# Kernel optimization log

Measured on AMD Instinct MI355X. Metric: run time of the kernel, lower is better.

The kernel has to match this reference:

```python
import jax, jax.numpy as jnp
import numpy as np

SAMPLE_RATE = 44100
NUM_FILTERS = 3
FREQ_LO, FREQ_HI = 100.0, 3000.0
Q_LO, Q_HI = 1.0, 5.0
GAIN_LO, GAIN_HI = -24.0, 24.0


def _center_freqs():
    # power_ratio(i/N, f_lo, f_hi) = f_lo * (f_hi/f_lo)**(i/N)
    return [FREQ_LO * (FREQ_HI / FREQ_LO) ** (i / NUM_FILTERS) for i in range(NUM_FILTERS)]


def setup_inputs() -> dict:
    key = jax.random.key(0)
    k1, k2, k3 = jax.random.split(key, 3)
    audio = jax.random.normal(k1, (32, 441000), dtype=jnp.float32)  # [B, T]
    # Q sampled like power_ratio(u, q_lo, q_hi) = q_lo*(q_hi/q_lo)**u
    u = jax.random.uniform(k2, (NUM_FILTERS,), dtype=jnp.float32)
    qs = Q_LO * (Q_HI / Q_LO) ** u
    gains = jax.random.uniform(k3, (NUM_FILTERS,), dtype=jnp.float32,
                               minval=GAIN_LO, maxval=GAIN_HI)
    return {"audio": audio, "qs": qs, "gains": gains}


def _biquad(x, b0, b1, b2, a1, a2):
    """Direct-form-I biquad over time axis. x: [B, T]; coeffs normalized by a0."""
    B = x.shape[0]
    z = jnp.zeros((B,), x.dtype)

    def step(carry, xn):
        x1, x2, y1, y2 = carry
        yn = b0 * xn + b1 * x1 + b2 * x2 - a1 * y1 - a2 * y2
        return (xn, x1, yn, y1), yn

    _, y = jax.lax.scan(step, (z, z, z, z), x.T)  # scan over T
    return y.T


def _peaking_eq(audio, center_freq, gain, Q):
    # torchaudio.functional.equalizer_biquad coefficients
    w0 = 2.0 * jnp.pi * center_freq / SAMPLE_RATE
    alpha = jnp.sin(w0) / (2.0 * Q)
    A = jnp.exp(gain / 40.0 * jnp.log(10.0))  # 10**(gain/40)
    b0 = 1.0 + alpha * A
    b1 = -2.0 * jnp.cos(w0)
    b2 = 1.0 - alpha * A
    a0 = 1.0 + alpha / A
    a1 = -2.0 * jnp.cos(w0)
    a2 = 1.0 - alpha / A
    return _biquad(audio, b0 / a0, b1 / a0, b2 / a0, a1 / a0, a2 / a0)


def reference(audio, qs, gains):
    cfs = _center_freqs()
    for i in range(NUM_FILTERS):
        audio = _peaking_eq(audio, cfs[i], gains[i], qs[i])
    return audio
```

## Files before the change

### kernel.cpp

```cpp
#include <hip/hip_runtime.h>
#include <math.h>

#define SR      44100.0
#define T_LEN   441000
#define B_ROWS  32
#define NCH     13782
#define GCH     (B_ROWS * NCH)
#define BPR     54
#define NBLK    (B_ROWS * BPR)
#define NMAT    14

#define WS_MAT  0
#define WS_AG   512
#define WS_F    21248

typedef __attribute__((address_space(1))) const void gconst_t;
typedef __attribute__((address_space(3))) void lds_t;
#define GL2LDS(gp, lp) __builtin_amdgcn_global_load_lds((gconst_t*)(gp), (lds_t*)(lp), 16, 0, 0)


#define COMPUTE_COEFS(scoef, dco, qs, gains) do { \
    if (threadIdx.x < 3) { \
      int f = threadIdx.x; \
      double cfq = 100.0 * exp(log(30.0) * (double)f / 3.0); \
      double w0 = 2.0 * M_PI * cfq / SR; \
      double alpha = sin(w0) / (2.0 * (double)qs[f]); \
      double Ag = exp((double)gains[f] * (2.302585092994045684 / 40.0)); \
      double a0 = 1.0 + alpha / Ag; \
      double c0 = (1.0 + alpha * Ag) / a0; \
      double c1 = (-2.0 * cos(w0)) / a0; \
      double c2 = (1.0 - alpha * Ag) / a0; \
      double c3 = c1; \
      double c4 = (1.0 - alpha / Ag) / a0; \
      dco[f*5+0]=c0; dco[f*5+1]=c1; dco[f*5+2]=c2; dco[f*5+3]=c3; dco[f*5+4]=c4; \
      scoef[f*5+0]=(float)c0; scoef[f*5+1]=(float)c1; scoef[f*5+2]=(float)c2; \
      scoef[f*5+3]=(float)c3; scoef[f*5+4]=(float)c4; \
    } \
  } while (0)

#define LOAD_COEFS(cf) \
  const float b00=cf[0],b10=cf[1],b20=cf[2],a10=cf[3],a20=cf[4]; \
  const float b01=cf[5],b11=cf[6],b21=cf[7],a11=cf[8],a21=cf[9]; \
  const float b02=cf[10],b12=cf[11],b22=cf[12],a12=cf[13],a22=cf[14];

#define CASCADE_STEP(xx) do { \
    float y1 = fmaf(b00, (xx), s11); \
    s11 = fmaf(-a10, y1, fmaf(b10, (xx), s21)); \
    s21 = fmaf(-a20, y1, b20 * (xx)); \
    float y2 = fmaf(b01, y1, s12); \
    s12 = fmaf(-a11, y2, fmaf(b11, y1, s22)); \
    s22 = fmaf(-a21, y2, b21 * y1); \
    y3 = fmaf(b02, y2, s13); \
    s13 = fmaf(-a12, y3, fmaf(b12, y2, s23)); \
    s23 = fmaf(-a22, y3, b22 * y2); \
  } while (0)

#define MV6(dst, M, v, add) do { \
    _Pragma("unroll") \
    for (int _i = 0; _i < 6; _i++) { \
      float _s = (add)[_i]; \
      _Pragma("unroll") \
      for (int _k = 0; _k < 6; _k++) _s = fmaf((M)[_i*6+_k], (v)[_k], _s); \
      (dst)[_i] = _s; \
    } \
  } while (0)

__device__ __forceinline__ void mm6d(const double* X, const double* Y, double* Z, int t) {
  if (t < 36) {
    int i = t / 6, j = t % 6;
    double s = 0.0;
    #pragma unroll
    for (int k = 0; k < 6; k++) s += X[i*6+k] * Y[k*6+j];
    Z[t] = s;
  }
}


#define STAGE_AUDIO() do { \
    if (span4 == 512) { \
      _Pragma("unroll") \
      for (int i = 0; i < 8; i++) { \
        int s = (i << 6) + lane; \
        int g = (s & ~7) | ((s & 7) ^ ((s >> 3) & 7)); \
        GL2LDS(xp + g, slab + (i << 8)); \
      } \
    } else { \
      _Pragma("unroll") \
      for (int i = 0; i < 8; i++) { \
        int s = (i << 6) + lane; \
        int g = (s & ~7) | ((s & 7) ^ ((s >> 3) & 7)); \
        if (g < span4) GL2LDS(xp + g, slab + (i << 8)); \
      } \
    } \
  } while (0)


__global__ __launch_bounds__(256) void kA_scan(const float* __restrict__ x,
                                               const float* __restrict__ qs,
                                               const float* __restrict__ gains,
                                               float* __restrict__ ws) {
  __shared__ __align__(16) float lds[4 * 2048];
  __shared__ double Da[36], Db[36];
  __shared__ double dco[15];
  __shared__ float sVm[NMAT][36];
  __shared__ float scoef[16];
  const int tid = threadIdx.x;
  const int wib = tid >> 6, lane = tid & 63;
  const int b = blockIdx.x;
  const int row = b / BPR, jb = b - row * BPR;
  const int wci = (jb << 2) + wib;
  long rowbase = (long)row * T_LEN;
  int s0 = wci << 11;
  int span4 = (min(2048, T_LEN - s0)) >> 2;
  const float4* xp = (const float4*)(x + rowbase + s0);
  float* slab = lds + (wib << 11);
  STAGE_AUDIO();
  COMPUTE_COEFS(scoef, dco, qs, gains);
  if (wib == 0) {
    if (lane == 0) {
      double u[7] = {0,0,0,0,0,0,1};
      for (int f = 0; f < 3; f++) {
        double c0=dco[f*5+0], c1=dco[f*5+1], c2=dco[f*5+2], c3=dco[f*5+3], c4=dco[f*5+4];
        double yv[7], s1p[7], s2p[7];
        for (int i = 0; i < 7; i++) {
          yv[i]  = c0 * u[i] + ((i == 2*f)   ? 1.0 : 0.0);
          s1p[i] = c1 * u[i] + ((i == 2*f+1) ? 1.0 : 0.0) - c3 * yv[i];
          s2p[i] = c2 * u[i] - c4 * yv[i];
        }
        for (int i = 0; i < 6; i++) { Da[(2*f)*6+i] = s1p[i]; Da[(2*f+1)*6+i] = s2p[i]; }
        for (int i = 0; i < 7; i++) u[i] = yv[i];
      }
    }
    double* cur = Da; double* oth = Db;
    #pragma unroll
    for (int s = 0; s < 5; s++) {
      mm6d(cur, cur, oth, lane);
      double* tm = cur; cur = oth; oth = tm;
    }
    #pragma unroll
    for (int k = 0; k < NMAT; k++) {
      if (lane < 36) {
        float wv = (float)cur[lane];
        sVm[k][lane] = wv;
        if (b == 0) ws[WS_MAT + k*36 + lane] = wv;
      }
      if (k < NMAT - 1) {
        mm6d(cur, cur, oth, lane);
        double* tm = cur; cur = oth; oth = tm;
      }
    }
  }
  __syncthreads();

  int ci = (jb << 8) + tid;
  bool valid = ci < NCH;
  float f6[6] = {0,0,0,0,0,0};
  if (valid) {
    LOAD_COEFS(scoef);
    int n4 = (ci == NCH - 1) ? 2 : 8;
    const float* rowp = slab + (lane << 5);
    int xr = lane & 7;
    float s11=0,s21=0,s12=0,s22=0,s13=0,s23=0, y3;
    if (n4 == 8) {
      #pragma unroll
      for (int j4 = 0; j4 < 8; j4++) {
        float4 v = *(const float4*)(rowp + ((j4 ^ xr) << 2));
        CASCADE_STEP(v.x); CASCADE_STEP(v.y); CASCADE_STEP(v.z); CASCADE_STEP(v.w);
      }
    } else {
      for (int j4 = 0; j4 < 2; j4++) {
        float4 v = *(const float4*)(rowp + ((j4 ^ xr) << 2));
        CASCADE_STEP(v.x); CASCADE_STEP(v.y); CASCADE_STEP(v.z); CASCADE_STEP(v.w);
      }
    }
    (void)y3;
    f6[0]=s11; f6[1]=s21; f6[2]=s12; f6[3]=s22; f6[4]=s13; f6[5]=s23;
  }
  __syncthreads();

  float* src = lds;
  float* dst = lds + 1792;
  #pragma unroll
  for (int i = 0; i < 6; i++) src[tid*7 + i] = f6[i];
  __syncthreads();
  for (int k = 0; k < 8; k++) {
    int d = 1 << k;
    float nv[6];
    if (tid >= d) { MV6(nv, sVm[k], src + (tid-d)*7, src + tid*7); }
    else {
      #pragma unroll
      for (int i = 0; i < 6; i++) nv[i] = src[tid*7 + i];
    }
    #pragma unroll
    for (int i = 0; i < 6; i++) dst[tid*7 + i] = nv[i];
    __syncthreads();
    float* tm = src; src = dst; dst = tm;
  }
  if (valid) {
    float e[6];
    if (tid > 0) {
      #pragma unroll
      for (int i = 0; i < 6; i++) e[i] = src[(tid-1)*7 + i];
    } else {
      #pragma unroll
      for (int i = 0; i < 6; i++) e[i] = 0.0f;
    }
    float2* E = (float2*)(ws + WS_F + ((long)row * NCH + ci) * 6);
    E[0] = make_float2(e[0], e[1]); E[1] = make_float2(e[2], e[3]); E[2] = make_float2(e[4], e[5]);
  }
  if (tid == 255 && jb < BPR - 1) {
    #pragma unroll
    for (int i = 0; i < 6; i++) ws[WS_AG + ((long)row * BPR + jb) * 6 + i] = src[255*7 + i];
  }
}


__global__ __launch_bounds__(256) void kC_emit(const float* __restrict__ x,
                                               const float* __restrict__ qs,
                                               const float* __restrict__ gains,
                                               float* __restrict__ y,
                                               const float* __restrict__ ws) {
  __shared__ __align__(16) float lds[4 * 2048];
  __shared__ float smat[NMAT * 36];
  __shared__ float scoef[16];
  __shared__ double dco[15];
  __shared__ float sO[6];
  const int tid = threadIdx.x;
  const int wib = tid >> 6, lane = tid & 63;
  const int b = blockIdx.x;
  const int row = b / BPR, jb = b - row * BPR;
  const int wci = (jb << 2) + wib;
  long rowbase = (long)row * T_LEN;
  int s0 = wci << 11;
  int span4 = (min(2048, T_LEN - s0)) >> 2;
  const float4* xp = (const float4*)(x + rowbase + s0);
  float* slab = lds + (wib << 11);
  STAGE_AUDIO();
  for (int i = tid; i < NMAT * 36; i += 256) smat[i] = ws[WS_MAT + i];
  float ag[6] = {0,0,0,0,0,0};
  if (wib == 0 && lane < BPR - 1) {
    const float* p = ws + WS_AG + ((long)row * BPR + lane) * 6;
    #pragma unroll
    for (int i = 0; i < 6; i++) ag[i] = p[i];
  }
  COMPUTE_COEFS(scoef, dco, qs, gains);
  if (tid == 0 && jb == 0) {
    #pragma unroll
    for (int i = 0; i < 6; i++) sO[i] = 0.0f;
  }
  int ci = (jb << 8) + tid;
  bool valid = ci < NCH;
  float e0=0,e1v=0,e2=0,e3=0,e4=0,e5=0;
  if (valid) {
    const float2* E = (const float2*)(ws + WS_F + ((long)row * NCH + ci) * 6);
    float2 p0 = E[0], p1 = E[1], p2 = E[2];
    e0=p0.x; e1v=p0.y; e2=p1.x; e3=p1.y; e4=p2.x; e5=p2.y;
  }
  __syncthreads();

  if (wib == 0 && jb > 0) {
    float v6s[6];
    #pragma unroll
    for (int i = 0; i < 6; i++) v6s[i] = ag[i];
    #pragma unroll
    for (int k = 0; k < 6; k++) {
      int d = 1 << k;
      float u[6];
      #pragma unroll
      for (int i = 0; i < 6; i++) u[i] = __shfl_up(v6s[i], d, 64);
      float nv[6];
      MV6(nv, smat + (8 + k) * 36, u, v6s);
      #pragma unroll
      for (int i = 0; i < 6; i++) v6s[i] = (lane >= d) ? nv[i] : v6s[i];
    }
    if (lane == jb - 1) {
      #pragma unroll
      for (int i = 0; i < 6; i++) sO[i] = v6s[i];
    }
  }
  __syncthreads();

  if (valid) {
    LOAD_COEFS(scoef);
    float m[6];
    #pragma unroll
    for (int i = 0; i < 6; i++) m[i] = sO[i];
    float z6[6] = {0,0,0,0,0,0};
    #pragma unroll
    for (int k = 0; k < 8; k++) {
      if ((tid >> k) & 1) {
        float nm[6];
        MV6(nm, smat + k*36, m, z6);
        #pragma unroll
        for (int i = 0; i < 6; i++) m[i] = nm[i];
      }
    }
    float s11=e0+m[0], s21=e1v+m[1], s12=e2+m[2], s22=e3+m[3], s13=e4+m[4], s23=e5+m[5];
    int n4 = (ci == NCH - 1) ? 2 : 8;
    float* rowp = slab + (lane << 5);
    int xr = lane & 7;
    float y3;
    if (n4 == 8) {
      #pragma unroll
      for (int j4 = 0; j4 < 8; j4++) {
        float* p = rowp + ((j4 ^ xr) << 2);
        float4 v = *(const float4*)p;
        float4 o;
        CASCADE_STEP(v.x); o.x = y3;
        CASCADE_STEP(v.y); o.y = y3;
        CASCADE_STEP(v.z); o.z = y3;
        CASCADE_STEP(v.w); o.w = y3;
        *(float4*)p = o;
      }
    } else {
      for (int j4 = 0; j4 < 2; j4++) {
        float* p = rowp + ((j4 ^ xr) << 2);
        float4 v = *(const float4*)p;
        float4 o;
        CASCADE_STEP(v.x); o.x = y3;
        CASCADE_STEP(v.y); o.y = y3;
        CASCADE_STEP(v.z); o.z = y3;
        CASCADE_STEP(v.w); o.w = y3;
        *(float4*)p = o;
      }
    }
  }
  __syncthreads();
  float4* yp = (float4*)(y + rowbase + s0);
  if (span4 == 512) {
    #pragma unroll
    for (int i = 0; i < 8; i++) {
      int g = (i << 6) + lane;
      int s = (g & ~7) | ((g & 7) ^ ((g >> 3) & 7));
      yp[g] = *(const float4*)(slab + (s << 2));
    }
  } else {
    #pragma unroll
    for (int i = 0; i < 8; i++) {
      int g = (i << 6) + lane;
      int s = (g & ~7) | ((g & 7) ^ ((g >> 3) & 7));
      if (g < span4) yp[g] = *(const float4*)(slab + (s << 2));
    }
  }
}

extern "C" void kernel_launch(void* const* d_in, const int* in_sizes, int n_in,
                              void* d_out, int out_size, void* d_ws, size_t ws_size,
                              hipStream_t stream) {
  const float* audio = (const float*)d_in[0];
  const float* qs    = (const float*)d_in[1];
  const float* gains = (const float*)d_in[2];
  float* out = (float*)d_out;
  float* ws  = (float*)d_ws;

  hipLaunchKernelGGL(kA_scan, dim3(NBLK), dim3(256), 0, stream, audio, qs, gains, ws);
  hipLaunchKernelGGL(kC_emit, dim3(NBLK), dim3(256), 0, stream, audio, qs, gains, out, ws);
}
```

Measured before the change: 59.96 us.

## Drop block barriers via per-wave coefficients and shorten the intra-block scan

Each wave now computes its own copy of the biquad coefficients. This lets the block-wide barrier after setup in the scan kernel become a per-wave vmcnt wait. The block scan runs 7 doubling steps instead of 8, and the last carry is applied with one extra matrix-vector product per thread for the upper half. In the emit kernel, the cross-block carry scan is merged into the setup phase, removing one __syncthreads. The trade-off is redundant coefficient math per wave and a correctness dependence on sVm being ready before the next barrier.

```diff
diff --git a/kernel.cpp b/kernel.cpp
--- a/kernel.cpp
+++ b/kernel.cpp
@@ -19,9 +19,9 @@
 #define GL2LDS(gp, lp) __builtin_amdgcn_global_load_lds((gconst_t*)(gp), (lds_t*)(lp), 16, 0, 0)
 
 
-#define COMPUTE_COEFS(scoef, dco, qs, gains) do { \
-    if (threadIdx.x < 3) { \
-      int f = threadIdx.x; \
+#define COMPUTE_COEFS_WAVE(scoef4, dco_opt) do { \
+    if (lane < 3) { \
+      int f = lane; \
       double cfq = 100.0 * exp(log(30.0) * (double)f / 3.0); \
       double w0 = 2.0 * M_PI * cfq / SR; \
       double alpha = sin(w0) / (2.0 * (double)qs[f]); \
@@ -32,9 +32,11 @@
       double c2 = (1.0 - alpha * Ag) / a0; \
       double c3 = c1; \
       double c4 = (1.0 - alpha / Ag) / a0; \
-      dco[f*5+0]=c0; dco[f*5+1]=c1; dco[f*5+2]=c2; dco[f*5+3]=c3; dco[f*5+4]=c4; \
-      scoef[f*5+0]=(float)c0; scoef[f*5+1]=(float)c1; scoef[f*5+2]=(float)c2; \
-      scoef[f*5+3]=(float)c3; scoef[f*5+4]=(float)c4; \
+      double* _d = (double*)(dco_opt); \
+      if (_d && wib == 0) { _d[f*5+0]=c0; _d[f*5+1]=c1; _d[f*5+2]=c2; _d[f*5+3]=c3; _d[f*5+4]=c4; } \
+      float* _sc = (scoef4) + (wib << 4); \
+      _sc[f*5+0]=(float)c0; _sc[f*5+1]=(float)c1; _sc[f*5+2]=(float)c2; \
+      _sc[f*5+3]=(float)c3; _sc[f*5+4]=(float)c4; \
     } \
   } while (0)
 
@@ -102,8 +104,8 @@
   __shared__ __align__(16) float lds[4 * 2048];
   __shared__ double Da[36], Db[36];
   __shared__ double dco[15];
-  __shared__ float sVm[NMAT][36];
-  __shared__ float scoef[16];
+  __shared__ float sVm[8][36];
+  __shared__ float scoef4[64];
   const int tid = threadIdx.x;
   const int wib = tid >> 6, lane = tid & 63;
   const int b = blockIdx.x;
@@ -115,7 +117,7 @@
   const float4* xp = (const float4*)(x + rowbase + s0);
   float* slab = lds + (wib << 11);
   STAGE_AUDIO();
-  COMPUTE_COEFS(scoef, dco, qs, gains);
+  COMPUTE_COEFS_WAVE(scoef4, dco);
   if (wib == 0) {
     if (lane == 0) {
       double u[7] = {0,0,0,0,0,0,1};
@@ -141,7 +143,7 @@
     for (int k = 0; k < NMAT; k++) {
       if (lane < 36) {
         float wv = (float)cur[lane];
-        sVm[k][lane] = wv;
+        if (k < 8) sVm[k][lane] = wv;
         if (b == 0) ws[WS_MAT + k*36 + lane] = wv;
       }
       if (k < NMAT - 1) {
@@ -150,13 +152,14 @@
       }
     }
   }
-  __syncthreads();
+  asm volatile("s_waitcnt vmcnt(0)" ::: "memory");
 
   int ci = (jb << 8) + tid;
   bool valid = ci < NCH;
   float f6[6] = {0,0,0,0,0,0};
   if (valid) {
-    LOAD_COEFS(scoef);
+    const float* cf = scoef4 + (wib << 4);
+    LOAD_COEFS(cf);
     int n4 = (ci == NCH - 1) ? 2 : 8;
     const float* rowp = slab + (lane << 5);
     int xr = lane & 7;
@@ -183,7 +186,7 @@
   #pragma unroll
   for (int i = 0; i < 6; i++) src[tid*7 + i] = f6[i];
   __syncthreads();
-  for (int k = 0; k < 8; k++) {
+  for (int k = 0; k < 7; k++) {
     int d = 1 << k;
     float nv[6];
     if (tid >= d) { MV6(nv, sVm[k], src + (tid-d)*7, src + tid*7); }
@@ -198,19 +201,23 @@
   }
   if (valid) {
     float e[6];
-    if (tid > 0) {
+    if (tid == 0) {
+      #pragma unroll
+      for (int i = 0; i < 6; i++) e[i] = 0.0f;
+    } else if (tid <= 128) {
       #pragma unroll
       for (int i = 0; i < 6; i++) e[i] = src[(tid-1)*7 + i];
     } else {
-      #pragma unroll
-      for (int i = 0; i < 6; i++) e[i] = 0.0f;
+      MV6(e, sVm[7], src + (tid-129)*7, src + (tid-1)*7);
     }
     float2* E = (float2*)(ws + WS_F + ((long)row * NCH + ci) * 6);
     E[0] = make_float2(e[0], e[1]); E[1] = make_float2(e[2], e[3]); E[2] = make_float2(e[4], e[5]);
   }
   if (tid == 255 && jb < BPR - 1) {
-    #pragma unroll
-    for (int i = 0; i < 6; i++) ws[WS_AG + ((long)row * BPR + jb) * 6 + i] = src[255*7 + i];
+    float g6[6];
+    MV6(g6, sVm[7], src + 126*7 + 7, src + 255*7);
+    #pragma unroll
+    for (int i = 0; i < 6; i++) ws[WS_AG + ((long)row * BPR + jb) * 6 + i] = g6[i];
   }
 }
 
@@ -221,9 +228,9 @@
                                                float* __restrict__ y,
                                                const float* __restrict__ ws) {
   __shared__ __align__(16) float lds[4 * 2048];
-  __shared__ float smat[NMAT * 36];
-  __shared__ float scoef[16];
-  __shared__ double dco[15];
+  __shared__ float smat[8 * 36];
+  __shared__ float sB[6 * 36];
+  __shared__ float scoef4[64];
   __shared__ float sO[6];
   const int tid = threadIdx.x;
   const int wib = tid >> 6, lane = tid & 63;
@@ -236,18 +243,8 @@
   const float4* xp = (const float4*)(x + rowbase + s0);
   float* slab = lds + (wib << 11);
   STAGE_AUDIO();
-  for (int i = tid; i < NMAT * 36; i += 256) smat[i] = ws[WS_MAT + i];
-  float ag[6] = {0,0,0,0,0,0};
-  if (wib == 0 && lane < BPR - 1) {
-    const float* p = ws + WS_AG + ((long)row * BPR + lane) * 6;
-    #pragma unroll
-    for (int i = 0; i < 6; i++) ag[i] = p[i];
-  }
-  COMPUTE_COEFS(scoef, dco, qs, gains);
-  if (tid == 0 && jb == 0) {
-    #pragma unroll
-    for (int i = 0; i < 6; i++) sO[i] = 0.0f;
-  }
+  for (int i = tid; i < 8 * 36; i += 256) smat[i] = ws[WS_MAT + i];
+  COMPUTE_COEFS_WAVE(scoef4, (double*)nullptr);
   int ci = (jb << 8) + tid;
   bool valid = ci < NCH;
   float e0=0,e1v=0,e2=0,e3=0,e4=0,e5=0;
@@ -256,32 +253,45 @@
     float2 p0 = E[0], p1 = E[1], p2 = E[2];
     e0=p0.x; e1v=p0.y; e2=p1.x; e3=p1.y; e4=p2.x; e5=p2.y;
   }
+  if (wib == 0) {
+    for (int i = lane; i < 6 * 36; i += 64) sB[i] = ws[WS_MAT + 8 * 36 + i];
+    float ag[6] = {0,0,0,0,0,0};
+    if (lane < BPR - 1) {
+      const float* p = ws + WS_AG + ((long)row * BPR + lane) * 6;
+      #pragma unroll
+      for (int i = 0; i < 6; i++) ag[i] = p[i];
+    }
+    if (jb == 0) {
+      if (lane == 0) {
+        #pragma unroll
+        for (int i = 0; i < 6; i++) sO[i] = 0.0f;
+      }
+    } else {
+      float v6s[6];
+      #pragma unroll
+      for (int i = 0; i < 6; i++) v6s[i] = ag[i];
+      #pragma unroll
+      for (int k = 0; k < 6; k++) {
+        int d = 1 << k;
+        float u[6];
+        #pragma unroll
+        for (int i = 0; i < 6; i++) u[i] = __shfl_up(v6s[i], d, 64);
+        float nv[6];
+        MV6(nv, sB + k * 36, u, v6s);
+        #pragma unroll
+        for (int i = 0; i < 6; i++) v6s[i] = (lane >= d) ? nv[i] : v6s[i];
+      }
+      if (lane == jb - 1) {
+        #pragma unroll
+        for (int i = 0; i < 6; i++) sO[i] = v6s[i];
+      }
+    }
+  }
   __syncthreads();
 
-  if (wib == 0 && jb > 0) {
-    float v6s[6];
-    #pragma unroll
-    for (int i = 0; i < 6; i++) v6s[i] = ag[i];
-    #pragma unroll
-    for (int k = 0; k < 6; k++) {
-      int d = 1 << k;
-      float u[6];
-      #pragma unroll
-      for (int i = 0; i < 6; i++) u[i] = __shfl_up(v6s[i], d, 64);
-      float nv[6];
-      MV6(nv, smat + (8 + k) * 36, u, v6s);
-      #pragma unroll
-      for (int i = 0; i < 6; i++) v6s[i] = (lane >= d) ? nv[i] : v6s[i];
-    }
-    if (lane == jb - 1) {
-      #pragma unroll
-      for (int i = 0; i < 6; i++) sO[i] = v6s[i];
-    }
-  }
-  __syncthreads();
-
   if (valid) {
-    LOAD_COEFS(scoef);
+    const float* cf = scoef4 + (wib << 4);
+    LOAD_COEFS(cf);
     float m[6];
     #pragma unroll
     for (int i = 0; i < 6; i++) m[i] = sO[i];
```

Result: slower. 65.52 us (+9.3%).

## Drop block barrier before cascade, compute per-wave coefficients, trim matrix powers

Applied to the files above, without the earlier changes.

Each wave now computes its own copy of the biquad coefficients into a per-wave LDS slot. The block-wide barrier before the per-chunk cascade is replaced with a per-wave wait on its own async global-to-LDS loads. This lets waves 1-3 start filtering without waiting for wave 0's double-precision matrix power chain. Blocks other than block 0 now compute only the 8 matrix powers they use instead of 14. The risk is that later consumers of sVm must still be ordered by a later barrier.

```diff
diff --git a/kernel.cpp b/kernel.cpp
--- a/kernel.cpp
+++ b/kernel.cpp
@@ -38,6 +38,26 @@
     } \
   } while (0)
 
+#define COMPUTE_COEFS_PW(scoef4, dco) do { \
+    if (lane < 3) { \
+      int f = lane; \
+      double cfq = 100.0 * exp(log(30.0) * (double)f / 3.0); \
+      double w0 = 2.0 * M_PI * cfq / SR; \
+      double alpha = sin(w0) / (2.0 * (double)qs[f]); \
+      double Ag = exp((double)gains[f] * (2.302585092994045684 / 40.0)); \
+      double a0 = 1.0 + alpha / Ag; \
+      double c0 = (1.0 + alpha * Ag) / a0; \
+      double c1 = (-2.0 * cos(w0)) / a0; \
+      double c2 = (1.0 - alpha * Ag) / a0; \
+      double c3 = c1; \
+      double c4 = (1.0 - alpha / Ag) / a0; \
+      if (wib == 0) { dco[f*5+0]=c0; dco[f*5+1]=c1; dco[f*5+2]=c2; dco[f*5+3]=c3; dco[f*5+4]=c4; } \
+      float* _sc = (scoef4) + (wib << 4); \
+      _sc[f*5+0]=(float)c0; _sc[f*5+1]=(float)c1; _sc[f*5+2]=(float)c2; \
+      _sc[f*5+3]=(float)c3; _sc[f*5+4]=(float)c4; \
+    } \
+  } while (0)
+
 #define LOAD_COEFS(cf) \
   const float b00=cf[0],b10=cf[1],b20=cf[2],a10=cf[3],a20=cf[4]; \
   const float b01=cf[5],b11=cf[6],b21=cf[7],a11=cf[8],a21=cf[9]; \
@@ -102,8 +122,8 @@
   __shared__ __align__(16) float lds[4 * 2048];
   __shared__ double Da[36], Db[36];
   __shared__ double dco[15];
-  __shared__ float sVm[NMAT][36];
-  __shared__ float scoef[16];
+  __shared__ float sVm[8][36];
+  __shared__ float scoef4[64];
   const int tid = threadIdx.x;
   const int wib = tid >> 6, lane = tid & 63;
   const int b = blockIdx.x;
@@ -115,7 +135,7 @@
   const float4* xp = (const float4*)(x + rowbase + s0);
   float* slab = lds + (wib << 11);
   STAGE_AUDIO();
-  COMPUTE_COEFS(scoef, dco, qs, gains);
+  COMPUTE_COEFS_PW(scoef4, dco);
   if (wib == 0) {
     if (lane == 0) {
       double u[7] = {0,0,0,0,0,0,1};
@@ -137,26 +157,27 @@
       mm6d(cur, cur, oth, lane);
       double* tm = cur; cur = oth; oth = tm;
     }
-    #pragma unroll
-    for (int k = 0; k < NMAT; k++) {
+    const int kmax = (b == 0) ? NMAT : 8;
+    for (int k = 0; k < kmax; k++) {
       if (lane < 36) {
         float wv = (float)cur[lane];
-        sVm[k][lane] = wv;
+        if (k < 8) sVm[k][lane] = wv;
         if (b == 0) ws[WS_MAT + k*36 + lane] = wv;
       }
-      if (k < NMAT - 1) {
+      if (k < kmax - 1) {
         mm6d(cur, cur, oth, lane);
         double* tm = cur; cur = oth; oth = tm;
       }
     }
   }
-  __syncthreads();
+  asm volatile("s_waitcnt vmcnt(0)" ::: "memory");
 
   int ci = (jb << 8) + tid;
   bool valid = ci < NCH;
   float f6[6] = {0,0,0,0,0,0};
   if (valid) {
-    LOAD_COEFS(scoef);
+    const float* cf = scoef4 + (wib << 4);
+    LOAD_COEFS(cf);
     int n4 = (ci == NCH - 1) ? 2 : 8;
     const float* rowp = slab + (lane << 5);
     int xr = lane & 7;
```

New measurement: 58.64 us (median of 2 runs). 2.2% less time.
